# Optimization experiments

Hardware: AMD Instinct MI355X
Metric: run time of the kernel (lower is better)

## Reference

```python
import jax, jax.numpy as jnp
import numpy as np

B, T, F, H = 64, 512, 128, 512
NUM_LAYERS = 3


def _lstm_layer(x_tbf, W_ih, W_hh, b_ih, b_hh):
    # x_tbf: [T, B, in], W_ih: [4H, in], W_hh: [4H, H]
    # PyTorch gate order: i, f, g, o
    Hd = W_hh.shape[1]
    Bd = x_tbf.shape[1]
    # precompute input projections for all timesteps (one big GEMM)
    x_proj = jnp.einsum('tbf,gf->tbg', x_tbf, W_ih) + b_ih  # [T, B, 4H]

    def step(carry, xp_t):
        h, c = carry
        gates = xp_t + h @ W_hh.T + b_hh  # [B, 4H]
        i, f, g, o = jnp.split(gates, 4, axis=-1)
        i = jax.nn.sigmoid(i)
        f = jax.nn.sigmoid(f)
        g = jnp.tanh(g)
        o = jax.nn.sigmoid(o)
        c = f * c + i * g
        h = o * jnp.tanh(c)
        return (h, c), h

    h0 = jnp.zeros((Bd, Hd), x_tbf.dtype)
    c0 = jnp.zeros((Bd, Hd), x_tbf.dtype)
    _, hs = jax.lax.scan(step, (h0, c0), x_proj)
    return hs  # [T, B, H]


def setup_inputs() -> dict:
    key = jax.random.key(0)
    ks = jax.random.split(key, 20)
    s = 1.0 / np.sqrt(H)
    inp = {"input_tensor": jax.random.normal(ks[0], (B, T, F), jnp.float32)}
    in_dims = [F, H, H]
    ki = 1
    for l in range(NUM_LAYERS):
        inp[f"W_ih{l}"] = jax.random.uniform(ks[ki], (4 * H, in_dims[l]), jnp.float32, -s, s); ki += 1
        inp[f"W_hh{l}"] = jax.random.uniform(ks[ki], (4 * H, H), jnp.float32, -s, s); ki += 1
        inp[f"b_ih{l}"] = jax.random.uniform(ks[ki], (4 * H,), jnp.float32, -s, s); ki += 1
        inp[f"b_hh{l}"] = jax.random.uniform(ks[ki], (4 * H,), jnp.float32, -s, s); ki += 1
    s1 = 1.0 / np.sqrt(H)
    inp["fc_W1"] = jax.random.uniform(ks[13], (64, H), jnp.float32, -s1, s1)
    inp["fc_b1"] = jax.random.uniform(ks[14], (64,), jnp.float32, -s1, s1)
    s2 = 1.0 / np.sqrt(64)
    inp["fc_W2"] = jax.random.uniform(ks[15], (1, 64), jnp.float32, -s2, s2)
    inp["fc_b2"] = jax.random.uniform(ks[16], (1,), jnp.float32, -s2, s2)
    return inp


def reference(input_tensor, W_ih0, W_hh0, b_ih0, b_hh0,
              W_ih1, W_hh1, b_ih1, b_hh1,
              W_ih2, W_hh2, b_ih2, b_hh2,
              fc_W1, fc_b1, fc_W2, fc_b2):
    x = jnp.transpose(input_tensor, (1, 0, 2))  # [T, B, F]
    x = _lstm_layer(x, W_ih0, W_hh0, b_ih0, b_hh0)
    x = _lstm_layer(x, W_ih1, W_hh1, b_ih1, b_hh1)  # eval mode: no dropout
    x = _lstm_layer(x, W_ih2, W_hh2, b_ih2, b_hh2)
    last = x[-1]  # [B, H]
    h1 = jax.nn.relu(last @ fc_W1.T + fc_b1)
    out = jax.nn.relu(h1 @ fc_W2.T + fc_b2)  # [B, 1]
    return out
```

## Files before the change

### kernel.cpp

```cpp
#include <hip/hip_runtime.h>
#include <hip/hip_fp16.h>
#include <math.h>

#define B_ 64
#define T_ 512
#define F_ 128
#define H_ 512
#define NBLK 96
#define SPIN_MAX (1 << 23)

typedef _Float16 f16x8 __attribute__((ext_vector_type(8)));
typedef float f32x4 __attribute__((ext_vector_type(4)));
typedef int   i32x4 __attribute__((ext_vector_type(4)));

__device__ __forceinline__ unsigned short f2h(float f) {
    return __half_as_ushort(__float2half(f));
}
__device__ __forceinline__ float h2f(unsigned short u) {
    return __half2float(__ushort_as_half(u));
}

__global__ void transpose_x(const float* __restrict__ in, unsigned* __restrict__ xs) {
    const int t = blockIdx.x;
    for (int idx = threadIdx.x; idx < B_ * F_ / 4; idx += blockDim.x) {
        const int kp2 = idx >> 6;
        const int bb = idx & 63;
        const float* src = in + (size_t)bb * T_ * F_ + (size_t)t * F_ + 4 * kp2;
        const unsigned h0 = f2h(src[0]), h1 = f2h(src[1]);
        const unsigned h2 = f2h(src[2]), h3 = f2h(src[3]);
        const unsigned dw0 = h0 | (h1 << 16);
        const unsigned dw1 = h2 | (h3 << 16);
        *(unsigned long long*)(xs + (size_t)t * 4096 + (size_t)kp2 * 128 + bb * 2) =
            ((unsigned long long)dw1 << 32) | dw0;
    }
}

__device__ __forceinline__ float sigmoid_(float x) {
    return __builtin_amdgcn_rcpf(1.0f + __expf(-x));
}
__device__ __forceinline__ float tanh_(float x) {
    return 1.0f - 2.0f * __builtin_amdgcn_rcpf(1.0f + __expf(2.0f * x));
}

__device__ __forceinline__ unsigned long long loadc_u64(const unsigned* p) {
    return __hip_atomic_load((const unsigned long long*)p, __ATOMIC_RELAXED,
                             __HIP_MEMORY_SCOPE_AGENT);
}
__device__ __forceinline__ unsigned loadc_u32(const unsigned* p) {
    return __hip_atomic_load(p, __ATOMIC_RELAXED, __HIP_MEMORY_SCOPE_AGENT);
}
__device__ __forceinline__ void storec_u64(unsigned* p, unsigned long long v) {
    __hip_atomic_store((unsigned long long*)p, v, __ATOMIC_RELAXED,
                       __HIP_MEMORY_SCOPE_AGENT);
}
__device__ __forceinline__ void storec_f(float* p, float v) {
    __hip_atomic_store(p, v, __ATOMIC_RELAXED, __HIP_MEMORY_SCOPE_AGENT);
}
__device__ __forceinline__ float loadc_f(const float* p) {
    return __hip_atomic_load(p, __ATOMIC_RELAXED, __HIP_MEMORY_SCOPE_AGENT);
}

__device__ __forceinline__ void gbar(int* __restrict__ slots, int bid, int tid, int e) {
    asm volatile("s_waitcnt vmcnt(0) lgkmcnt(0)" ::: "memory");
    __syncthreads();
    if (tid == 0)
        __hip_atomic_store(&slots[bid * 16], e, __ATOMIC_RELAXED,
                           __HIP_MEMORY_SCOPE_AGENT);
    if (tid < NBLK) {
        int guard = 0;
        while (__hip_atomic_load(&slots[tid * 16], __ATOMIC_RELAXED,
                                 __HIP_MEMORY_SCOPE_AGENT) < e &&
               ++guard < SPIN_MAX)
            __builtin_amdgcn_s_sleep(1);
    }
    __syncthreads();
}

template <int NKX, bool XCOH>
__device__ __forceinline__ void step_mfma(const unsigned* __restrict__ xs_l,
                                          const unsigned* __restrict__ hs_l,
                                          const unsigned short* wfrag,
                                          const int lane, f32x4 (&acc)[4]) {
    constexpr int NK = NKX + 16;
    constexpr int PD = 16;
    unsigned long long v[PD][2];

    auto load2 = [&](unsigned long long* d, int i) {
        const unsigned* p = (i < NKX) ? (xs_l + (size_t)i * 1024)
                                      : (hs_l + (size_t)(i - NKX) * 1024);
        if ((i < NKX) ? XCOH : true) {
            d[0] = loadc_u64(p);
            d[1] = loadc_u64(p + 128);
        } else {
            d[0] = *(const unsigned long long*)p;
            d[1] = *(const unsigned long long*)(p + 128);
        }
    };

#pragma unroll
    for (int p = 0; p < PD; ++p) load2(v[p], p);

#pragma unroll
    for (int i = 0; i < NK; ++i) {
        union Frag { i32x4 i4; f16x8 s; } Bf, A0, A1, A2, A3;
        const unsigned long long* d = v[i % PD];
        Bf.i4[0] = (int)(unsigned)d[0];
        Bf.i4[1] = (int)(unsigned)(d[0] >> 32);
        Bf.i4[2] = (int)(unsigned)d[1];
        Bf.i4[3] = (int)(unsigned)(d[1] >> 32);
        if (i + PD < NK) load2(v[i % PD], i + PD);
        A0.i4 = *(const i32x4*)&wfrag[i * 2048 + lane * 8];
        A1.i4 = *(const i32x4*)&wfrag[i * 2048 + 512 + lane * 8];
        A2.i4 = *(const i32x4*)&wfrag[i * 2048 + 1024 + lane * 8];
        A3.i4 = *(const i32x4*)&wfrag[i * 2048 + 1536 + lane * 8];
        acc[0] = __builtin_amdgcn_mfma_f32_16x16x32_f16(A0.s, Bf.s, acc[0], 0, 0, 0);
        acc[1] = __builtin_amdgcn_mfma_f32_16x16x32_f16(A1.s, Bf.s, acc[1], 0, 0, 0);
        acc[2] = __builtin_amdgcn_mfma_f32_16x16x32_f16(A2.s, Bf.s, acc[2], 0, 0, 0);
        acc[3] = __builtin_amdgcn_mfma_f32_16x16x32_f16(A3.s, Bf.s, acc[3], 0, 0, 0);
    }
}

__global__ void __launch_bounds__(256, 1) lstm_scan(
    const unsigned* __restrict__ xs, unsigned* __restrict__ hb,
    float* __restrict__ h1s, float* __restrict__ out,
    int* __restrict__ bar_slots, int* __restrict__ bar_go,
    const float* __restrict__ Wih0, const float* __restrict__ Whh0,
    const float* __restrict__ bih0, const float* __restrict__ bhh0,
    const float* __restrict__ Wih1, const float* __restrict__ Whh1,
    const float* __restrict__ bih1, const float* __restrict__ bhh1,
    const float* __restrict__ Wih2, const float* __restrict__ Whh2,
    const float* __restrict__ bih2, const float* __restrict__ bhh2,
    const float* __restrict__ fcW1, const float* __restrict__ fcb1,
    const float* __restrict__ fcW2, const float* __restrict__ fcb2) {
    __shared__ unsigned short wfrag[32 * 2048];
    __shared__ float redsc[4 * 64];

    const float* WihA[3] = {Wih0, Wih1, Wih2};
    const float* WhhA[3] = {Whh0, Whh1, Whh2};
    const float* bihA[3] = {bih0, bih1, bih2};
    const float* bhhA[3] = {bhh0, bhh1, bhh2};

    const int tid   = threadIdx.x;
    const int bid   = blockIdx.x;
    const int layer = bid >> 5;
    const int cb    = bid & 31;
    const int c0    = cb * 16;
    const int lane  = tid & 63;
    const int w     = __builtin_amdgcn_readfirstlane(tid >> 6);
    const int KX    = (layer == 0) ? F_ : H_;
    const int NK    = KX / 32 + 16;

    const float* wih = WihA[layer];
    const float* whh = WhhA[layer];

    for (int idx = tid; idx < NK * 2048; idx += 256) {
        const int i = idx >> 11, rem = idx & 2047;
        const int rg = rem >> 9, r2 = rem & 511;
        const int l = r2 >> 3, j = r2 & 7;
        const int m = l & 15;
        const int grow = (m & 3) * 512 + c0 + rg * 4 + (m >> 2);
        const int k = i * 32 + (l >> 4) * 8 + j;
        const float f = (k < KX) ? wih[(size_t)grow * KX + k]
                                 : whh[(size_t)grow * 512 + (k - KX)];
        wfrag[i * 2048 + rg * 512 + l * 8 + j] = f2h(f);
    }
    __syncthreads();

    const int fb    = w * 16 + (lane & 15);
    const int q     = lane >> 4;
    float bias[4][4];
#pragma unroll
    for (int rg = 0; rg < 4; ++rg)
#pragma unroll
        for (int g = 0; g < 4; ++g)
            bias[rg][g] = bihA[layer][g * 512 + c0 + rg * 4 + q] +
                          bhhA[layer][g * 512 + c0 + rg * 4 + q];

    unsigned* hb_l = hb + (size_t)layer * 32768;
    const unsigned* hb_in = hb + (size_t)(layer - 1) * 32768;
    int hstore[4];
#pragma unroll
    for (int rg = 0; rg < 4; ++rg)
        hstore[rg] = (cb * 4 + rg) * 128 + fb * 2;

    float c_reg[4] = {0.0f, 0.0f, 0.0f, 0.0f};
    const int laneoff = q * 256 + fb * 2;

    for (int s = 0; s < T_ + 2; ++s) {
        const int t = s - layer;
        if (t >= 0 && t < T_) {
            const int p_out  = t & 1;
            const int p_prev = (t + 1) & 1;
            const unsigned* xs_l =
                ((layer == 0) ? (xs + (size_t)t * 4096)
                              : (hb_in + (size_t)p_out * 16384)) + laneoff;
            const unsigned* hs_l = hb_l + (size_t)p_prev * 16384 + laneoff;

            f32x4 acc[4] = {{0.f,0.f,0.f,0.f},{0.f,0.f,0.f,0.f},
                            {0.f,0.f,0.f,0.f},{0.f,0.f,0.f,0.f}};
            if (layer == 0) step_mfma<4, false>(xs_l, hs_l, wfrag, lane, acc);
            else            step_mfma<16, true>(xs_l, hs_l, wfrag, lane, acc);

#pragma unroll
            for (int rg = 0; rg < 4; ++rg) {
                float a[4];
#pragma unroll
                for (int g = 0; g < 4; ++g)
                    a[g] = bias[rg][g] + acc[rg][g];

                const float ig = sigmoid_(a[0]);
                const float fg = sigmoid_(a[1]);
                const float gg = tanh_(a[2]);
                const float og = sigmoid_(a[3]);
                c_reg[rg] = fg * c_reg[rg] + ig * gg;
                const float hv = og * tanh_(c_reg[rg]);

                const unsigned P0 = (unsigned)f2h(hv);
                const unsigned P1 = (unsigned)__shfl_xor((int)P0, 16, 64) & 0xFFFFu;
                const unsigned D  = P0 | (P1 << 16);
                const unsigned D2 = (unsigned)__shfl_xor((int)D, 32, 64);
                if (q == 0) {
                    storec_u64(&hb_l[(size_t)p_out * 16384 + hstore[rg]],
                               ((unsigned long long)D2 << 32) | D);
                }
            }
        }
        gbar(bar_slots, bid, tid, s + 1);
    }

    const unsigned* h2u = hb + (size_t)2 * 32768 + 16384;
    const int fcb = tid & 63;
    if (bid < 64) {
        float part = 0.0f;
        const float* wrow = fcW1 + (size_t)bid * H_ + w * 128;
#pragma unroll 8
        for (int k = 0; k < 128; ++k) {
            const int kk = w * 128 + k;
            const unsigned dv =
                loadc_u32(h2u + (kk >> 2) * 128 + fcb * 2 + ((kk >> 1) & 1));
            const float val = h2f((unsigned short)((dv >> ((kk & 1) * 16)) & 0xFFFFu));
            part = fmaf(wrow[k], val, part);
        }
        redsc[w * 64 + fcb] = part;
        __syncthreads();
        if (tid < 64) {
            float acc2 = fcb1[bid] + redsc[tid] + redsc[64 + tid] +
                         redsc[128 + tid] + redsc[192 + tid];
            storec_f(&h1s[bid * B_ + tid], fmaxf(acc2, 0.0f));
        }
    }
    gbar(bar_slots, bid, tid, T_ + 3);
    if (bid == 0 && tid < 64) {
        float acc2 = fcb2[0];
#pragma unroll
        for (int c = 0; c < 64; ++c)
            acc2 = fmaf(fcW2[c], loadc_f(&h1s[c * B_ + tid]), acc2);
        out[tid] = fmaxf(acc2, 0.0f);
    }
}

extern "C" void kernel_launch(void* const* d_in, const int* in_sizes, int n_in,
                              void* d_out, int out_size, void* d_ws, size_t ws_size,
                              hipStream_t stream) {
    const float* in    = (const float*)d_in[0];
    const float* Wih0  = (const float*)d_in[1];
    const float* Whh0  = (const float*)d_in[2];
    const float* bih0  = (const float*)d_in[3];
    const float* bhh0  = (const float*)d_in[4];
    const float* Wih1  = (const float*)d_in[5];
    const float* Whh1  = (const float*)d_in[6];
    const float* bih1  = (const float*)d_in[7];
    const float* bhh1  = (const float*)d_in[8];
    const float* Wih2  = (const float*)d_in[9];
    const float* Whh2  = (const float*)d_in[10];
    const float* bih2  = (const float*)d_in[11];
    const float* bhh2  = (const float*)d_in[12];
    const float* fcW1  = (const float*)d_in[13];
    const float* fcb1  = (const float*)d_in[14];
    const float* fcW2  = (const float*)d_in[15];
    const float* fcb2  = (const float*)d_in[16];
    float* outp = (float*)d_out;

    unsigned* xs  = (unsigned*)d_ws;
    unsigned* hbf = xs + (size_t)T_ * 4096;
    float*    h1s = (float*)(hbf + (size_t)3 * 32768);
    int*      bar = (int*)(h1s + 64 * 64);
    int*      bar_slots = bar;
    int*      bar_go    = bar + NBLK * 16;

    hipMemsetAsync(hbf, 0,
                   ((size_t)3 * 32768 + 64 * 64 + NBLK * 16 + 16) * sizeof(int),
                   stream);

    transpose_x<<<dim3(T_), dim3(256), 0, stream>>>(in, xs);

    void* args[] = {
        (void*)&xs, (void*)&hbf, (void*)&h1s, (void*)&outp,
        (void*)&bar_slots, (void*)&bar_go,
        (void*)&Wih0, (void*)&Whh0, (void*)&bih0, (void*)&bhh0,
        (void*)&Wih1, (void*)&Whh1, (void*)&bih1, (void*)&bhh1,
        (void*)&Wih2, (void*)&Whh2, (void*)&bih2, (void*)&bhh2,
        (void*)&fcW1, (void*)&fcb1, (void*)&fcW2, (void*)&fcb2};
    hipLaunchCooperativeKernel((void*)lstm_scan, dim3(NBLK), dim3(256), args, 0, stream);
}
```

Measured before the change: 2.620 ms.

## Replace global barrier with per-wave flag dataflow sync and 4-deep h ring buffers

Swaps the grid-wide barrier after each wavefront step for per-wave progress flags. Each layer polls only its own layer's flags (recurrent dependency), its producer layer's flags (input ready), and its consumer layer's flags (to avoid overwriting a buffer still being read). Hidden-state buffers grow from double to 4-deep ring buffers so layers can drift apart by several timesteps. The goal is to remove lockstep barrier latency and let the layers pipeline loosely. The cost is more flag polling traffic and a shorter spin timeout, which risks silent wrong results if a wait times out.

```diff
diff --git a/kernel.cpp b/kernel.cpp
--- a/kernel.cpp
+++ b/kernel.cpp
@@ -7,7 +7,7 @@
 #define F_ 128
 #define H_ 512
 #define NBLK 96
-#define SPIN_MAX (1 << 23)
+#define SPIN_MAX (1 << 18)
 
 typedef _Float16 f16x8 __attribute__((ext_vector_type(8)));
 typedef float f32x4 __attribute__((ext_vector_type(4)));
@@ -59,71 +59,135 @@
 __device__ __forceinline__ float loadc_f(const float* p) {
     return __hip_atomic_load(p, __ATOMIC_RELAXED, __HIP_MEMORY_SCOPE_AGENT);
 }
-
-__device__ __forceinline__ void gbar(int* __restrict__ slots, int bid, int tid, int e) {
-    asm volatile("s_waitcnt vmcnt(0) lgkmcnt(0)" ::: "memory");
-    __syncthreads();
-    if (tid == 0)
-        __hip_atomic_store(&slots[bid * 16], e, __ATOMIC_RELAXED,
-                           __HIP_MEMORY_SCOPE_AGENT);
-    if (tid < NBLK) {
-        int guard = 0;
-        while (__hip_atomic_load(&slots[tid * 16], __ATOMIC_RELAXED,
-                                 __HIP_MEMORY_SCOPE_AGENT) < e &&
-               ++guard < SPIN_MAX)
-            __builtin_amdgcn_s_sleep(1);
-    }
-    __syncthreads();
-}
-
-template <int NKX, bool XCOH>
-__device__ __forceinline__ void step_mfma(const unsigned* __restrict__ xs_l,
-                                          const unsigned* __restrict__ hs_l,
-                                          const unsigned short* wfrag,
-                                          const int lane, f32x4 (&acc)[4]) {
-    constexpr int NK = NKX + 16;
-    constexpr int PD = 16;
-    unsigned long long v[PD][2];
-
-    auto load2 = [&](unsigned long long* d, int i) {
-        const unsigned* p = (i < NKX) ? (xs_l + (size_t)i * 1024)
-                                      : (hs_l + (size_t)(i - NKX) * 1024);
-        if ((i < NKX) ? XCOH : true) {
-            d[0] = loadc_u64(p);
-            d[1] = loadc_u64(p + 128);
-        } else {
-            d[0] = *(const unsigned long long*)p;
-            d[1] = *(const unsigned long long*)(p + 128);
-        }
-    };
-
-#pragma unroll
-    for (int p = 0; p < PD; ++p) load2(v[p], p);
-
-#pragma unroll
-    for (int i = 0; i < NK; ++i) {
-        union Frag { i32x4 i4; f16x8 s; } Bf, A0, A1, A2, A3;
-        const unsigned long long* d = v[i % PD];
-        Bf.i4[0] = (int)(unsigned)d[0];
-        Bf.i4[1] = (int)(unsigned)(d[0] >> 32);
-        Bf.i4[2] = (int)(unsigned)d[1];
-        Bf.i4[3] = (int)(unsigned)(d[1] >> 32);
-        if (i + PD < NK) load2(v[i % PD], i + PD);
-        A0.i4 = *(const i32x4*)&wfrag[i * 2048 + lane * 8];
-        A1.i4 = *(const i32x4*)&wfrag[i * 2048 + 512 + lane * 8];
-        A2.i4 = *(const i32x4*)&wfrag[i * 2048 + 1024 + lane * 8];
-        A3.i4 = *(const i32x4*)&wfrag[i * 2048 + 1536 + lane * 8];
-        acc[0] = __builtin_amdgcn_mfma_f32_16x16x32_f16(A0.s, Bf.s, acc[0], 0, 0, 0);
-        acc[1] = __builtin_amdgcn_mfma_f32_16x16x32_f16(A1.s, Bf.s, acc[1], 0, 0, 0);
-        acc[2] = __builtin_amdgcn_mfma_f32_16x16x32_f16(A2.s, Bf.s, acc[2], 0, 0, 0);
-        acc[3] = __builtin_amdgcn_mfma_f32_16x16x32_f16(A3.s, Bf.s, acc[3], 0, 0, 0);
+__device__ __forceinline__ int loadc_i(const int* p) {
+    return __hip_atomic_load(p, __ATOMIC_RELAXED, __HIP_MEMORY_SCOPE_AGENT);
+}
+__device__ __forceinline__ void storec_i(int* p, int v) {
+    __hip_atomic_store(p, v, __ATOMIC_RELAXED, __HIP_MEMORY_SCOPE_AGENT);
+}
+
+__device__ __forceinline__ void poll128(const int* __restrict__ base, int need,
+                                        int lane) {
+    int g = 0;
+    for (;;) {
+        const bool ok = (loadc_i(base + lane * 32) >= need) &&
+                        (loadc_i(base + (lane + 64) * 32) >= need);
+        if (__all(ok)) return;
+        if (++g >= SPIN_MAX) return;
+        __builtin_amdgcn_s_sleep(1);
+    }
+}
+
+template <int NKX, bool XPLAIN, bool HASPROD, bool HASWAR>
+__device__ void scan_layer(
+    const unsigned* __restrict__ xb,
+    unsigned* __restrict__ hbuf,
+    const int* __restrict__ fl_self, const int* __restrict__ fl_prod,
+    const int* __restrict__ fl_cons, int* __restrict__ fl_mine,
+    const unsigned short* __restrict__ wfrag, const float (&bias)[4][4],
+    const int (&hstore)[4], int lane, int q, int laneoff) {
+    float c_reg[4] = {0.f, 0.f, 0.f, 0.f};
+    int prod_seen = 0, self_seen = 0, war_seen = 0;
+    union Frag { i32x4 i4; f16x8 s; };
+
+    for (int t = 0; t < T_; ++t) {
+        if (HASPROD && prod_seen < t + 1) {
+            poll128(fl_prod, t + 1, lane);
+            prod_seen = t + 1;
+        }
+        unsigned long long vx[NKX][2], vh[16][2];
+        const unsigned* xsrc = XPLAIN ? (xb + (size_t)t * 4096 + laneoff)
+                                      : (xb + (size_t)(t & 3) * 16384 + laneoff);
+#pragma unroll
+        for (int i = 0; i < NKX; ++i) {
+            if (XPLAIN) {
+                vx[i][0] = *(const unsigned long long*)(xsrc + i * 1024);
+                vx[i][1] = *(const unsigned long long*)(xsrc + i * 1024 + 128);
+            } else {
+                vx[i][0] = loadc_u64(xsrc + i * 1024);
+                vx[i][1] = loadc_u64(xsrc + i * 1024 + 128);
+            }
+        }
+        if (self_seen < t) {
+            poll128(fl_self, t, lane);
+            self_seen = t;
+        }
+        const unsigned* hs = hbuf + (size_t)((t + 3) & 3) * 16384 + laneoff;
+#pragma unroll
+        for (int j = 0; j < 16; ++j) {
+            vh[j][0] = loadc_u64(hs + j * 1024);
+            vh[j][1] = loadc_u64(hs + j * 1024 + 128);
+        }
+
+        f32x4 acc[4] = {{0.f,0.f,0.f,0.f},{0.f,0.f,0.f,0.f},
+                        {0.f,0.f,0.f,0.f},{0.f,0.f,0.f,0.f}};
+#pragma unroll
+        for (int i = 0; i < NKX; ++i) {
+            Frag Bf, A0, A1, A2, A3;
+            Bf.i4[0] = (int)(unsigned)vx[i][0];
+            Bf.i4[1] = (int)(unsigned)(vx[i][0] >> 32);
+            Bf.i4[2] = (int)(unsigned)vx[i][1];
+            Bf.i4[3] = (int)(unsigned)(vx[i][1] >> 32);
+            A0.i4 = *(const i32x4*)&wfrag[i * 2048 + lane * 8];
+            A1.i4 = *(const i32x4*)&wfrag[i * 2048 + 512 + lane * 8];
+            A2.i4 = *(const i32x4*)&wfrag[i * 2048 + 1024 + lane * 8];
+            A3.i4 = *(const i32x4*)&wfrag[i * 2048 + 1536 + lane * 8];
+            acc[0] = __builtin_amdgcn_mfma_f32_16x16x32_f16(A0.s, Bf.s, acc[0], 0, 0, 0);
+            acc[1] = __builtin_amdgcn_mfma_f32_16x16x32_f16(A1.s, Bf.s, acc[1], 0, 0, 0);
+            acc[2] = __builtin_amdgcn_mfma_f32_16x16x32_f16(A2.s, Bf.s, acc[2], 0, 0, 0);
+            acc[3] = __builtin_amdgcn_mfma_f32_16x16x32_f16(A3.s, Bf.s, acc[3], 0, 0, 0);
+        }
+#pragma unroll
+        for (int j = 0; j < 16; ++j) {
+            Frag Bf, A0, A1, A2, A3;
+            Bf.i4[0] = (int)(unsigned)vh[j][0];
+            Bf.i4[1] = (int)(unsigned)(vh[j][0] >> 32);
+            Bf.i4[2] = (int)(unsigned)vh[j][1];
+            Bf.i4[3] = (int)(unsigned)(vh[j][1] >> 32);
+            const int i = NKX + j;
+            A0.i4 = *(const i32x4*)&wfrag[i * 2048 + lane * 8];
+            A1.i4 = *(const i32x4*)&wfrag[i * 2048 + 512 + lane * 8];
+            A2.i4 = *(const i32x4*)&wfrag[i * 2048 + 1024 + lane * 8];
+            A3.i4 = *(const i32x4*)&wfrag[i * 2048 + 1536 + lane * 8];
+            acc[0] = __builtin_amdgcn_mfma_f32_16x16x32_f16(A0.s, Bf.s, acc[0], 0, 0, 0);
+            acc[1] = __builtin_amdgcn_mfma_f32_16x16x32_f16(A1.s, Bf.s, acc[1], 0, 0, 0);
+            acc[2] = __builtin_amdgcn_mfma_f32_16x16x32_f16(A2.s, Bf.s, acc[2], 0, 0, 0);
+            acc[3] = __builtin_amdgcn_mfma_f32_16x16x32_f16(A3.s, Bf.s, acc[3], 0, 0, 0);
+        }
+
+        if (HASWAR && t >= 4 && war_seen < t - 3) {
+            poll128(fl_cons, t - 3, lane);
+            war_seen = t - 3;
+        }
+
+#pragma unroll
+        for (int rg = 0; rg < 4; ++rg) {
+            float a[4];
+#pragma unroll
+            for (int g = 0; g < 4; ++g) a[g] = bias[rg][g] + acc[rg][g];
+            const float ig = sigmoid_(a[0]);
+            const float fg = sigmoid_(a[1]);
+            const float gg = tanh_(a[2]);
+            const float og = sigmoid_(a[3]);
+            c_reg[rg] = fg * c_reg[rg] + ig * gg;
+            const float hv = og * tanh_(c_reg[rg]);
+            const unsigned P0 = (unsigned)f2h(hv);
+            const unsigned P1 = (unsigned)__shfl_xor((int)P0, 16, 64) & 0xFFFFu;
+            const unsigned D  = P0 | (P1 << 16);
+            const unsigned D2 = (unsigned)__shfl_xor((int)D, 32, 64);
+            if (q == 0)
+                storec_u64(hbuf + (size_t)(t & 3) * 16384 + hstore[rg],
+                           ((unsigned long long)D2 << 32) | D);
+        }
+        asm volatile("s_waitcnt vmcnt(0) lgkmcnt(0)" ::: "memory");
+        if (lane == 0) storec_i(fl_mine, t + 1);
     }
 }
 
 __global__ void __launch_bounds__(256, 1) lstm_scan(
-    const unsigned* __restrict__ xs, unsigned* __restrict__ hb,
+    const unsigned* __restrict__ xs, unsigned* __restrict__ hbf,
+    int* __restrict__ fli, int* __restrict__ fcf,
     float* __restrict__ h1s, float* __restrict__ out,
-    int* __restrict__ bar_slots, int* __restrict__ bar_go,
     const float* __restrict__ Wih0, const float* __restrict__ Whh0,
     const float* __restrict__ bih0, const float* __restrict__ bhh0,
     const float* __restrict__ Wih1, const float* __restrict__ Whh1,
@@ -166,8 +230,8 @@
     }
     __syncthreads();
 
-    const int fb    = w * 16 + (lane & 15);
-    const int q     = lane >> 4;
+    const int fb = w * 16 + (lane & 15);
+    const int q  = lane >> 4;
     float bias[4][4];
 #pragma unroll
     for (int rg = 0; rg < 4; ++rg)
@@ -176,61 +240,36 @@
             bias[rg][g] = bihA[layer][g * 512 + c0 + rg * 4 + q] +
                           bhhA[layer][g * 512 + c0 + rg * 4 + q];
 
-    unsigned* hb_l = hb + (size_t)layer * 32768;
-    const unsigned* hb_in = hb + (size_t)(layer - 1) * 32768;
     int hstore[4];
 #pragma unroll
-    for (int rg = 0; rg < 4; ++rg)
-        hstore[rg] = (cb * 4 + rg) * 128 + fb * 2;
-
-    float c_reg[4] = {0.0f, 0.0f, 0.0f, 0.0f};
+    for (int rg = 0; rg < 4; ++rg) hstore[rg] = (cb * 4 + rg) * 128 + fb * 2;
     const int laneoff = q * 256 + fb * 2;
 
-    for (int s = 0; s < T_ + 2; ++s) {
-        const int t = s - layer;
-        if (t >= 0 && t < T_) {
-            const int p_out  = t & 1;
-            const int p_prev = (t + 1) & 1;
-            const unsigned* xs_l =
-                ((layer == 0) ? (xs + (size_t)t * 4096)
-                              : (hb_in + (size_t)p_out * 16384)) + laneoff;
-            const unsigned* hs_l = hb_l + (size_t)p_prev * 16384 + laneoff;
-
-            f32x4 acc[4] = {{0.f,0.f,0.f,0.f},{0.f,0.f,0.f,0.f},
-                            {0.f,0.f,0.f,0.f},{0.f,0.f,0.f,0.f}};
-            if (layer == 0) step_mfma<4, false>(xs_l, hs_l, wfrag, lane, acc);
-            else            step_mfma<16, true>(xs_l, hs_l, wfrag, lane, acc);
-
-#pragma unroll
-            for (int rg = 0; rg < 4; ++rg) {
-                float a[4];
-#pragma unroll
-                for (int g = 0; g < 4; ++g)
-                    a[g] = bias[rg][g] + acc[rg][g];
-
-                const float ig = sigmoid_(a[0]);
-                const float fg = sigmoid_(a[1]);
-                const float gg = tanh_(a[2]);
-                const float og = sigmoid_(a[3]);
-                c_reg[rg] = fg * c_reg[rg] + ig * gg;
-                const float hv = og * tanh_(c_reg[rg]);
-
-                const unsigned P0 = (unsigned)f2h(hv);
-                const unsigned P1 = (unsigned)__shfl_xor((int)P0, 16, 64) & 0xFFFFu;
-                const unsigned D  = P0 | (P1 << 16);
-                const unsigned D2 = (unsigned)__shfl_xor((int)D, 32, 64);
-                if (q == 0) {
-                    storec_u64(&hb_l[(size_t)p_out * 16384 + hstore[rg]],
-                               ((unsigned long long)D2 << 32) | D);
-                }
-            }
-        }
-        gbar(bar_slots, bid, tid, s + 1);
-    }
-
-    const unsigned* h2u = hb + (size_t)2 * 32768 + 16384;
+    unsigned* hbuf = hbf + (size_t)layer * 4 * 16384;
+    const unsigned* xb =
+        (layer == 0) ? xs : (hbf + (size_t)(layer - 1) * 4 * 16384);
+    const int* fl_self = fli + layer * 128 * 32;
+    const int* fl_prod = fli + (layer > 0 ? layer - 1 : 0) * 128 * 32;
+    const int* fl_cons = fli + (layer < 2 ? layer + 1 : 2) * 128 * 32;
+    int* fl_mine = fli + (layer * 128 + cb * 4 + w) * 32;
+
+    if (layer == 0)
+        scan_layer<4, true, false, true>(xb, hbuf, fl_self, fl_prod, fl_cons,
+                                         fl_mine, wfrag, bias, hstore, lane, q,
+                                         laneoff);
+    else if (layer == 1)
+        scan_layer<16, false, true, true>(xb, hbuf, fl_self, fl_prod, fl_cons,
+                                          fl_mine, wfrag, bias, hstore, lane, q,
+                                          laneoff);
+    else
+        scan_layer<16, false, true, false>(xb, hbuf, fl_self, fl_prod, fl_cons,
+                                           fl_mine, wfrag, bias, hstore, lane,
+                                           q, laneoff);
+
+    const unsigned* h2u = hbf + (size_t)2 * 4 * 16384 + (size_t)3 * 16384;
     const int fcb = tid & 63;
     if (bid < 64) {
+        poll128(fli + 2 * 128 * 32, T_, lane);
         float part = 0.0f;
         const float* wrow = fcW1 + (size_t)bid * H_ + w * 128;
 #pragma unroll 8
@@ -248,14 +287,24 @@
                          redsc[128 + tid] + redsc[192 + tid];
             storec_f(&h1s[bid * B_ + tid], fmaxf(acc2, 0.0f));
         }
-    }
-    gbar(bar_slots, bid, tid, T_ + 3);
-    if (bid == 0 && tid < 64) {
-        float acc2 = fcb2[0];
-#pragma unroll
-        for (int c = 0; c < 64; ++c)
-            acc2 = fmaf(fcW2[c], loadc_f(&h1s[c * B_ + tid]), acc2);
-        out[tid] = fmaxf(acc2, 0.0f);
+        asm volatile("s_waitcnt vmcnt(0) lgkmcnt(0)" ::: "memory");
+        __syncthreads();
+        if (tid == 0) storec_i(&fcf[bid * 32], 1);
+    }
+    if (bid == 0) {
+        if (tid < 64) {
+            int g = 0;
+            while (loadc_i(&fcf[tid * 32]) < 1 && ++g < SPIN_MAX)
+                __builtin_amdgcn_s_sleep(1);
+        }
+        __syncthreads();
+        if (tid < 64) {
+            float acc2 = fcb2[0];
+#pragma unroll
+            for (int c = 0; c < 64; ++c)
+                acc2 = fmaf(fcW2[c], loadc_f(&h1s[c * B_ + tid]), acc2);
+            out[tid] = fmaxf(acc2, 0.0f);
+        }
     }
 }
 
@@ -283,20 +332,20 @@
 
     unsigned* xs  = (unsigned*)d_ws;
     unsigned* hbf = xs + (size_t)T_ * 4096;
-    float*    h1s = (float*)(hbf + (size_t)3 * 32768);
-    int*      bar = (int*)(h1s + 64 * 64);
-    int*      bar_slots = bar;
-    int*      bar_go    = bar + NBLK * 16;
+    int* fli = (int*)(hbf + (size_t)3 * 4 * 16384);
+    int* fcf = fli + 3 * 128 * 32;
+    float* h1s = (float*)(fcf + 64 * 32);
 
     hipMemsetAsync(hbf, 0,
-                   ((size_t)3 * 32768 + 64 * 64 + NBLK * 16 + 16) * sizeof(int),
+                   ((size_t)3 * 4 * 16384 + 3 * 128 * 32 + 64 * 32 + 64 * 64) *
+                       sizeof(int),
                    stream);
 
     transpose_x<<<dim3(T_), dim3(256), 0, stream>>>(in, xs);
 
     void* args[] = {
-        (void*)&xs, (void*)&hbf, (void*)&h1s, (void*)&outp,
-        (void*)&bar_slots, (void*)&bar_go,
+        (void*)&xs, (void*)&hbf, (void*)&fli, (void*)&fcf, (void*)&h1s,
+        (void*)&outp,
         (void*)&Wih0, (void*)&Whh0, (void*)&bih0, (void*)&bhh0,
         (void*)&Wih1, (void*)&Whh1, (void*)&bih1, (void*)&bhh1,
         (void*)&Wih2, (void*)&Whh2, (void*)&bih2, (void*)&bhh2,
```

Measured after the change: 3.296 ms. +25.8%, slower.
